# Kernel optimization log

Measured on AMD Instinct MI355X. Metric: run time of the kernel, lower is better.

## Reference

```python
import jax, jax.numpy as jnp
import numpy as np

EPS = 1e-5
NUM_GROUPS = 32
HT_MIN = -2.0
HT_MAX = 2.0


def setup_inputs() -> dict:
    key = jax.random.key(0)
    k1, k2 = jax.random.split(key)
    B, Cin, Cout, H, W = 32, 256, 512, 56, 56
    x = jax.random.normal(k1, (B, Cin, H, W), dtype=jnp.float32)
    weight = jax.random.normal(k2, (Cout, Cin), dtype=jnp.float32)
    gamma = jnp.ones((Cout,), dtype=jnp.float32)
    beta = jnp.zeros((Cout,), dtype=jnp.float32)
    return {"x": x, "weight": weight, "gamma": gamma, "beta": beta}


def reference(x, weight, gamma, beta) -> jnp.ndarray:
    B, Cin, H, W = x.shape
    Cout = weight.shape[0]
    G = NUM_GROUPS
    # 1x1-conv style GEMM over channels (no bias in the original kernel call)
    y = jnp.einsum("oc,bchw->bohw", weight, x)  # [B, Cout, H, W]
    # GroupNorm: stats over (channels-in-group, H, W) per sample
    yg = y.reshape(B, G, Cout // G, H, W)
    mean = jnp.mean(yg, axis=(2, 3, 4), keepdims=True)
    var = jnp.var(yg, axis=(2, 3, 4), keepdims=True)
    yn = ((yg - mean) * jax.lax.rsqrt(var + EPS)).reshape(B, Cout, H, W)
    yn = yn * gamma[None, :, None, None] + beta[None, :, None, None]
    # HardTanh clamp
    return jnp.clip(yn, HT_MIN, HT_MAX)
```

## Files before the change

### kernel.cpp

```cpp
#include <hip/hip_runtime.h>


#define HW    3136
#define CIN   256
#define COUT  512
#define BATCH 32
#define NG    32
#define CPG   16
#define EPS   1e-5f

typedef _Float16 f16x8 __attribute__((ext_vector_type(8)));
typedef float    f32x4 __attribute__((ext_vector_type(4)));
typedef unsigned int u32;

__device__ __forceinline__ void gload16(const void* g, void* l) {
  __builtin_amdgcn_global_load_lds(
      (const u32 __attribute__((address_space(1)))*)g,
      (u32 __attribute__((address_space(3)))*)l, 16, 0, 0);
}

__global__ __launch_bounds__(256) void k0_transpose(
    const float* __restrict__ x, const float* __restrict__ w,
    _Float16* __restrict__ xT, _Float16* __restrict__ wf)
{
  __shared__ float T[64 * 65];
  const int bid = blockIdx.x;
  const int t   = threadIdx.x;
  const int b   = bid / 196;
  const int r   = bid % 196;
  const int st  = r >> 2;
  const int ct  = r & 3;
  const int s0  = st * 64, c0 = ct * 64;

  const float* xb = x + ((size_t)b * CIN + c0) * HW + s0;
#pragma unroll
  for (int rr = 0; rr < 4; ++rr) {
    const int c_loc = (t >> 4) + rr * 16;
    const int s4    = (t & 15) * 4;
    const float4 v  = *(const float4*)(xb + (size_t)c_loc * HW + s4);
    T[(s4 + 0) * 65 + c_loc] = v.x;
    T[(s4 + 1) * 65 + c_loc] = v.y;
    T[(s4 + 2) * 65 + c_loc] = v.z;
    T[(s4 + 3) * 65 + c_loc] = v.w;
  }
  __syncthreads();
#pragma unroll
  for (int p = 0; p < 2; ++p) {
    const int s_loc = p * 32 + (t >> 3);
    const int cg    = (t & 7) * 8;
    f16x8 o;
#pragma unroll
    for (int j = 0; j < 8; ++j) o[j] = (_Float16)T[s_loc * 65 + cg + j];
    *(f16x8*)(xT + ((size_t)b * HW + s0 + s_loc) * CIN + c0 + cg) = o;
  }
  if (bid < (COUT * CIN) / 256) wf[bid * 256 + t] = (_Float16)w[bid * 256 + t];
}

__global__ __launch_bounds__(256) void k_gemm(
    const _Float16* __restrict__ xT, const _Float16* __restrict__ wf,
    float2* __restrict__ stats, _Float16* __restrict__ y)
{
  __shared__ __align__(16) _Float16 As[128 * 64];
  __shared__ __align__(16) _Float16 Bs[128 * 64];

  const int bid  = blockIdx.x;
  const int tile = (bid & 7) * 400 + (bid >> 3);
  const int mt   = tile & 3;
  const int q2   = tile >> 2;
  const int nt   = q2 % 25;
  const int b    = q2 / 25;
  const int s0   = (nt == 24) ? (HW - 128) : nt * 128;

  const int t    = threadIdx.x;
  const int lane = t & 63;
  const int wid  = t >> 6;
  const int wy   = wid >> 1, wx = wid & 1;
  const int lr   = lane >> 3;
  const int ccg  = (lane & 7) ^ lr;

  f32x4 acc[4][4] = {};
  const _Float16* xb = xT + (size_t)b * HW * CIN;

  for (int kt = 0; kt < 4; ++kt) {
    __syncthreads();
    const int ko = kt * 64;
#pragma unroll
    for (int u = 0; u < 4; ++u) {
      const int rowb = (wid * 4 + u) * 8 + lr;
      gload16(wf + (size_t)(mt * 128 + rowb) * CIN + ko + ccg * 8,
              As + (wid * 4 + u) * 512);
      gload16(xb + (size_t)(s0 + rowb) * CIN + ko + ccg * 8,
              Bs + (wid * 4 + u) * 512);
    }
    __syncthreads();
#pragma unroll
    for (int ks = 0; ks < 2; ++ks) {
      const int c = ks * 4 + (lane >> 4);
      f16x8 af[4], bfr[4];
#pragma unroll
      for (int mi = 0; mi < 4; ++mi) {
        const int m = wy * 64 + mi * 16 + (lane & 15);
        af[mi] = *(const f16x8*)(As + m * 64 + ((c ^ (m & 7)) * 8));
      }
#pragma unroll
      for (int ni = 0; ni < 4; ++ni) {
        const int n = wx * 64 + ni * 16 + (lane & 15);
        bfr[ni] = *(const f16x8*)(Bs + n * 64 + ((c ^ (n & 7)) * 8));
      }
#pragma unroll
      for (int mi = 0; mi < 4; ++mi)
#pragma unroll
        for (int ni = 0; ni < 4; ++ni)
          acc[mi][ni] = __builtin_amdgcn_mfma_f32_16x16x32_f16(
              af[mi], bfr[ni], acc[mi][ni], 0, 0, 0);
    }
  }

  const int slo  = (nt == 24) ? 3072 : 0;
  const int colb = s0 + wx * 64 + (lane & 15);
#pragma unroll
  for (int mi = 0; mi < 4; ++mi) {
    float s1 = 0.f, s2 = 0.f;
#pragma unroll
    for (int ni = 0; ni < 4; ++ni) {
      if (colb + ni * 16 >= slo) {
#pragma unroll
        for (int rr = 0; rr < 4; ++rr) {
          const float v = acc[mi][ni][rr];
          s1 += v; s2 += v * v;
        }
      }
    }
#pragma unroll
    for (int off = 32; off > 0; off >>= 1) {
      s1 += __shfl_down(s1, off, 64);
      s2 += __shfl_down(s2, off, 64);
    }
    if (lane == 0) {
      const int g = mt * 8 + wy * 4 + mi;
      stats[((b * NG + g) * 25 + nt) * 2 + wx] = make_float2(s1, s2);
    }
    const int row0 = mt * 128 + wy * 64 + mi * 16 + ((lane >> 4) << 2);
#pragma unroll
    for (int rr = 0; rr < 4; ++rr) {
      _Float16* yrow = y + ((size_t)b * COUT + row0 + rr) * HW + colb;
#pragma unroll
      for (int ni = 0; ni < 4; ++ni)
        if (colb + ni * 16 >= slo) yrow[ni * 16] = (_Float16)acc[mi][ni][rr];
    }
  }
}

__global__ __launch_bounds__(256) void k_finalize(
    const float2* __restrict__ stats, const float* __restrict__ gamma,
    const float* __restrict__ beta, float* __restrict__ ss)
{
  const int i = blockIdx.x * 256 + threadIdx.x;
  if (i < BATCH * COUT) {
    const int b  = i >> 9;
    const int co = i & (COUT - 1);
    const int g  = co >> 4;
    const float2* sp = stats + (size_t)(b * NG + g) * 50;
    float s1 = 0.f, s2 = 0.f;
#pragma unroll 10
    for (int j = 0; j < 50; ++j) { s1 += sp[j].x; s2 += sp[j].y; }
    const float cnt  = (float)(CPG * HW);
    const float mean = s1 / cnt;
    const float var  = s2 / cnt - mean * mean;
    const float rsig = rsqrtf(var + EPS);
    const float sc   = rsig * gamma[co];
    ss[i * 2 + 0] = sc;
    ss[i * 2 + 1] = beta[co] - mean * sc;
  }
}

__global__ __launch_bounds__(256) void k_norm(
    const _Float16* __restrict__ y, const float* __restrict__ ss,
    float* __restrict__ out)
{
  const u32 u   = blockIdx.x * 256 + threadIdx.x;
  const u32 row = u / (HW / 8);
  const u32 sp  = (u - row * (HW / 8)) * 8;
  const float sc = ss[row * 2 + 0];
  const float sh = ss[row * 2 + 1];
  const f16x8 v = *(const f16x8*)(y + (size_t)row * HW + sp);
  float4 o0, o1;
  o0.x = fminf(fmaxf((float)v[0] * sc + sh, -2.0f), 2.0f);
  o0.y = fminf(fmaxf((float)v[1] * sc + sh, -2.0f), 2.0f);
  o0.z = fminf(fmaxf((float)v[2] * sc + sh, -2.0f), 2.0f);
  o0.w = fminf(fmaxf((float)v[3] * sc + sh, -2.0f), 2.0f);
  o1.x = fminf(fmaxf((float)v[4] * sc + sh, -2.0f), 2.0f);
  o1.y = fminf(fmaxf((float)v[5] * sc + sh, -2.0f), 2.0f);
  o1.z = fminf(fmaxf((float)v[6] * sc + sh, -2.0f), 2.0f);
  o1.w = fminf(fmaxf((float)v[7] * sc + sh, -2.0f), 2.0f);
  float* op = out + (size_t)row * HW + sp;
  *(float4*)(op)     = o0;
  *(float4*)(op + 4) = o1;
}

extern "C" void kernel_launch(void* const* d_in, const int* in_sizes, int n_in,
                              void* d_out, int out_size, void* d_ws, size_t ws_size,
                              hipStream_t stream)
{
  const float* x     = (const float*)d_in[0];
  const float* w     = (const float*)d_in[1];
  const float* gamma = (const float*)d_in[2];
  const float* beta  = (const float*)d_in[3];
  float* out = (float*)d_out;

  const size_t xT_bytes = (size_t)BATCH * HW * CIN * 2;
  const size_t wf_bytes = (size_t)COUT * CIN * 2;
  const size_t st_bytes = (size_t)BATCH * NG * 50 * 8;
  const size_t ss_bytes = (size_t)BATCH * COUT * 2 * 4;
  const size_t y_bytes  = (size_t)BATCH * COUT * HW * 2;

  char* ws = (char*)d_ws;
  _Float16* xT = (_Float16*)ws;
  _Float16* wf = (_Float16*)(ws + xT_bytes);
  float2* stats = (float2*)(ws + xT_bytes + wf_bytes);
  float* ss    = (float*)(ws + xT_bytes + wf_bytes + st_bytes);
  _Float16* y  = (_Float16*)(ws + xT_bytes + wf_bytes + st_bytes + ss_bytes);

  if (ws_size < xT_bytes + wf_bytes + st_bytes + ss_bytes + y_bytes) return;

  k0_transpose<<<dim3(BATCH * 196), dim3(256), 0, stream>>>(x, w, xT, wf);
  k_gemm<<<dim3(BATCH * 100), dim3(256), 0, stream>>>(xT, wf, stats, y);
  k_finalize<<<dim3(BATCH * COUT / 256), dim3(256), 0, stream>>>(stats, gamma, beta, ss);
  k_norm<<<dim3(BATCH * COUT * HW / 8 / 256), dim3(256), 0, stream>>>(y, ss, out);
}
```

Measured before the change: 368.9 us.

## Double-buffer GEMM LDS tiles with K=32 stages and nontemporal output stores

The GEMM main loop now uses two LDS buffers with a K-step of 32. The next stage's global-to-LDS loads are issued before computing on the current buffer, overlapping memory with MFMA work and leaving one barrier per iteration. The swizzle changes to suit the 32-wide rows. Separately, the normalization kernel writes its float output with nontemporal stores to avoid polluting the cache. The tradeoffs are more loop iterations with smaller per-stage work and a possible LDS bank-conflict change.

Result: slower. 377.9 us (+2.4%).

```diff
diff --git a/kernel.cpp b/kernel.cpp
--- a/kernel.cpp
+++ b/kernel.cpp
@@ -60,8 +60,8 @@
     const _Float16* __restrict__ xT, const _Float16* __restrict__ wf,
     float2* __restrict__ stats, _Float16* __restrict__ y)
 {
-  __shared__ __align__(16) _Float16 As[128 * 64];
-  __shared__ __align__(16) _Float16 Bs[128 * 64];
+  __shared__ __align__(16) _Float16 As[2 * 128 * 32];
+  __shared__ __align__(16) _Float16 Bs[2 * 128 * 32];
 
   const int bid  = blockIdx.x;
   const int tile = (bid & 7) * 400 + (bid >> 3);
@@ -75,46 +75,58 @@
   const int lane = t & 63;
   const int wid  = t >> 6;
   const int wy   = wid >> 1, wx = wid & 1;
-  const int lr   = lane >> 3;
-  const int ccg  = (lane & 7) ^ lr;
+
+  const int r_st = t >> 2;
+  const int ch   = (t & 3) ^ ((r_st >> 1) & 3);
+
+  const _Float16* xb = xT + (size_t)b * HW * CIN;
+  const _Float16* gA0 = wf + (size_t)(mt * 128 + r_st) * CIN + ch * 8;
+  const _Float16* gA1 = gA0 + (size_t)64 * CIN;
+  const _Float16* gB0 = xb + (size_t)(s0 + r_st) * CIN + ch * 8;
+  const _Float16* gB1 = gB0 + (size_t)64 * CIN;
 
   f32x4 acc[4][4] = {};
-  const _Float16* xb = xT + (size_t)b * HW * CIN;
-
-  for (int kt = 0; kt < 4; ++kt) {
+
+#define STAGE(bufi, kt_)                                                  \
+  do {                                                                    \
+    gload16(gA0 + (kt_) * 32, As + (bufi) * 4096 + t * 8);                \
+    gload16(gA1 + (kt_) * 32, As + (bufi) * 4096 + 2048 + t * 8);         \
+    gload16(gB0 + (kt_) * 32, Bs + (bufi) * 4096 + t * 8);                \
+    gload16(gB1 + (kt_) * 32, Bs + (bufi) * 4096 + 2048 + t * 8);         \
+  } while (0)
+
+  STAGE(0, 0);
+  __syncthreads();
+
+  const int c = lane >> 4;
+#pragma unroll
+  for (int kt = 0; kt < 8; ++kt) {
+    const int cur = kt & 1;
+    if (kt < 7) STAGE(cur ^ 1, kt + 1);
+
+    f16x8 af[4], bfr[4];
+#pragma unroll
+    for (int mi = 0; mi < 4; ++mi) {
+      const int m = wy * 64 + mi * 16 + (lane & 15);
+      af[mi] = *(const f16x8*)(As + cur * 4096 + m * 32 +
+                               ((c ^ ((m >> 1) & 3)) * 8));
+    }
+#pragma unroll
+    for (int ni = 0; ni < 4; ++ni) {
+      const int n = wx * 64 + ni * 16 + (lane & 15);
+      bfr[ni] = *(const f16x8*)(Bs + cur * 4096 + n * 32 +
+                                ((c ^ ((n >> 1) & 3)) * 8));
+    }
+#pragma unroll
+    for (int mi = 0; mi < 4; ++mi)
+#pragma unroll
+      for (int ni = 0; ni < 4; ++ni)
+        acc[mi][ni] = __builtin_amdgcn_mfma_f32_16x16x32_f16(
+            af[mi], bfr[ni], acc[mi][ni], 0, 0, 0);
+
     __syncthreads();
-    const int ko = kt * 64;
-#pragma unroll
-    for (int u = 0; u < 4; ++u) {
-      const int rowb = (wid * 4 + u) * 8 + lr;
-      gload16(wf + (size_t)(mt * 128 + rowb) * CIN + ko + ccg * 8,
-              As + (wid * 4 + u) * 512);
-      gload16(xb + (size_t)(s0 + rowb) * CIN + ko + ccg * 8,
-              Bs + (wid * 4 + u) * 512);
-    }
-    __syncthreads();
-#pragma unroll
-    for (int ks = 0; ks < 2; ++ks) {
-      const int c = ks * 4 + (lane >> 4);
-      f16x8 af[4], bfr[4];
-#pragma unroll
-      for (int mi = 0; mi < 4; ++mi) {
-        const int m = wy * 64 + mi * 16 + (lane & 15);
-        af[mi] = *(const f16x8*)(As + m * 64 + ((c ^ (m & 7)) * 8));
-      }
-#pragma unroll
-      for (int ni = 0; ni < 4; ++ni) {
-        const int n = wx * 64 + ni * 16 + (lane & 15);
-        bfr[ni] = *(const f16x8*)(Bs + n * 64 + ((c ^ (n & 7)) * 8));
-      }
-#pragma unroll
-      for (int mi = 0; mi < 4; ++mi)
-#pragma unroll
-        for (int ni = 0; ni < 4; ++ni)
-          acc[mi][ni] = __builtin_amdgcn_mfma_f32_16x16x32_f16(
-              af[mi], bfr[ni], acc[mi][ni], 0, 0, 0);
-    }
-  }
+  }
+#undef STAGE
 
   const int slo  = (nt == 24) ? 3072 : 0;
   const int colb = s0 + wx * 64 + (lane & 15);
@@ -184,18 +196,18 @@
   const float sc = ss[row * 2 + 0];
   const float sh = ss[row * 2 + 1];
   const f16x8 v = *(const f16x8*)(y + (size_t)row * HW + sp);
-  float4 o0, o1;
-  o0.x = fminf(fmaxf((float)v[0] * sc + sh, -2.0f), 2.0f);
-  o0.y = fminf(fmaxf((float)v[1] * sc + sh, -2.0f), 2.0f);
-  o0.z = fminf(fmaxf((float)v[2] * sc + sh, -2.0f), 2.0f);
-  o0.w = fminf(fmaxf((float)v[3] * sc + sh, -2.0f), 2.0f);
-  o1.x = fminf(fmaxf((float)v[4] * sc + sh, -2.0f), 2.0f);
-  o1.y = fminf(fmaxf((float)v[5] * sc + sh, -2.0f), 2.0f);
-  o1.z = fminf(fmaxf((float)v[6] * sc + sh, -2.0f), 2.0f);
-  o1.w = fminf(fmaxf((float)v[7] * sc + sh, -2.0f), 2.0f);
+  f32x4 o0, o1;
+  o0[0] = fminf(fmaxf((float)v[0] * sc + sh, -2.0f), 2.0f);
+  o0[1] = fminf(fmaxf((float)v[1] * sc + sh, -2.0f), 2.0f);
+  o0[2] = fminf(fmaxf((float)v[2] * sc + sh, -2.0f), 2.0f);
+  o0[3] = fminf(fmaxf((float)v[3] * sc + sh, -2.0f), 2.0f);
+  o1[0] = fminf(fmaxf((float)v[4] * sc + sh, -2.0f), 2.0f);
+  o1[1] = fminf(fmaxf((float)v[5] * sc + sh, -2.0f), 2.0f);
+  o1[2] = fminf(fmaxf((float)v[6] * sc + sh, -2.0f), 2.0f);
+  o1[3] = fminf(fmaxf((float)v[7] * sc + sh, -2.0f), 2.0f);
   float* op = out + (size_t)row * HW + sp;
-  *(float4*)(op)     = o0;
-  *(float4*)(op + 4) = o1;
+  __builtin_nontemporal_store(o0, (f32x4*)(op));
+  __builtin_nontemporal_store(o1, (f32x4*)(op + 4));
 }
 
 extern "C" void kernel_launch(void* const* d_in, const int* in_sizes, int n_in,
```
